# Kernel tuning notes

Hardware: AMD Instinct MI355X
Metric: run time of the kernel (lower is better)

Reference implementation:

```python
import jax, jax.numpy as jnp
import numpy as np

N = 50000
E = 1_600_000


def spmm(edge_index, edge_weight, support, num_nodes):
    # adj[i, j] = w for (i=row, j=col); out[i] = sum_j adj[i,j] * support[j]
    row, col = edge_index[0], edge_index[1]
    msgs = support[col] * edge_weight[:, None]  # [E, d] gather + scale
    return jax.ops.segment_sum(msgs, row, num_segments=num_nodes)


def setup_inputs() -> dict:
    key = jax.random.key(0)
    ks = jax.random.split(key, 7)
    x = jax.random.normal(ks[0], (N, 128), dtype=jnp.float32)
    edge_index = jax.random.randint(ks[1], (2, E), 0, N, dtype=jnp.int64)
    edge_weight = jax.random.uniform(ks[2], (E,), dtype=jnp.float32)
    W1 = jax.random.normal(ks[3], (128, 128), dtype=jnp.float32) * (1.0 / np.sqrt(128))
    b1 = jax.random.normal(ks[4], (128,), dtype=jnp.float32) * (1.0 / np.sqrt(128))
    W2 = jax.random.normal(ks[5], (128, 40), dtype=jnp.float32) * (1.0 / np.sqrt(40))
    b2 = jax.random.normal(ks[6], (40,), dtype=jnp.float32) * (1.0 / np.sqrt(40))
    return {"x": x, "edge_index": edge_index, "edge_weight": edge_weight,
            "W1": W1, "b1": b1, "W2": W2, "b2": b2}


def reference(x, edge_index, edge_weight, W1, b1, W2, b2):
    n = x.shape[0]
    # layer 1: GraphConvolution + ReLU (dropout p=0.0 -> no-op)
    h = spmm(edge_index, edge_weight, x @ W1, n) + b1
    h = jax.nn.relu(h)
    # layer 2: GraphConvolution
    out = spmm(edge_index, edge_weight, h @ W2, n) + b2
    return jax.nn.log_softmax(out, axis=1)
```

## Files before the change

### kernel.cpp

```cpp
#include <hip/hip_runtime.h>
#include <hip/hip_fp16.h>
#include <math.h>

#define N_NODES 50000
#define N_EDGES 1600000
#define D1 128
#define D2 40
#define D2P 48
#define BROWS 128
#define NB 391
#define CHUNK 6250

typedef __attribute__((ext_vector_type(8))) short bf16x8;
typedef __attribute__((ext_vector_type(4))) float f32x4;

__device__ __forceinline__ void bf16_split(float v, unsigned short& h, unsigned short& l) {
    unsigned u = __float_as_uint(v);
    unsigned r = u + 0x7fffu + ((u >> 16) & 1u);
    h = (unsigned short)(r >> 16);
    float hf = __uint_as_float((unsigned)h << 16);
    float lof = v - hf;
    unsigned u2 = __float_as_uint(lof);
    unsigned r2 = u2 + 0x7fffu + ((u2 >> 16) & 1u);
    l = (unsigned short)(r2 >> 16);
}

__device__ __forceinline__ int edge_row(const unsigned int* ei, int e, int is64) {
    return (int)(is64 ? ei[2 * e] : ei[e]);
}
__device__ __forceinline__ int edge_col(const unsigned int* ei, int e, int is64) {
    return (int)(is64 ? ei[2 * (N_EDGES + e)] : ei[N_EDGES + e]);
}

__global__ __launch_bounds__(256) void setup_k(const unsigned int* __restrict__ ei,
                                               int* __restrict__ flag,
                                               unsigned int* __restrict__ gbhp,
                                               const float* __restrict__ W1,
                                               unsigned short* __restrict__ wh1,
                                               unsigned short* __restrict__ wl1,
                                               const float* __restrict__ W2,
                                               unsigned short* __restrict__ wh2,
                                               unsigned short* __restrict__ wl2) {
    int b = blockIdx.x, t = threadIdx.x;
    if (b == 0) {
        __shared__ int any;
        if (t == 0) any = 0;
        __syncthreads();
        for (int i = t; i < 2048; i += 256) {
            if (ei[2 * i + 1] != 0u) any = 1;
        }
        __syncthreads();
        if (t == 0) flag[0] = any ? 0 : 1;
    } else if (b <= 25) {
        int i = (b - 1) * 256 + t;
        if (i < NB * 16) gbhp[i] = 0u;
    } else if (b <= 89) {
        int idx = (b - 26) * 256 + t;
        int k = idx >> 7, n = idx & 127;
        unsigned short h, l;
        bf16_split(W1[k * 128 + n], h, l);
        int nt = n >> 4, ks = k >> 5;
        int lane = (n & 15) | (((k >> 3) & 3) << 4);
        int j = k & 7;
        int dst = ((nt * 4 + ks) * 64 + lane) * 8 + j;
        wh1[dst] = h;
        wl1[dst] = l;
    } else {
        int idx = (b - 90) * 256 + t;
        if (idx < 128 * D2P) {
            int k = idx / D2P, n = idx % D2P;
            float v = (n < D2) ? W2[k * D2 + n] : 0.f;
            unsigned short h, l;
            bf16_split(v, h, l);
            int nt = n >> 4, ks = k >> 5;
            int lane = (n & 15) | (((k >> 3) & 3) << 4);
            int j = k & 7;
            int dst = ((nt * 4 + ks) * 64 + lane) * 8 + j;
            wh2[dst] = h;
            wl2[dst] = l;
        }
    }
}

__global__ __launch_bounds__(256) void bhist_k(const unsigned int* __restrict__ ei,
                                               const int* __restrict__ flag,
                                               unsigned int* __restrict__ gbhp) {
    __shared__ unsigned int bh[NB];
    int is64 = flag[0];
    int t = threadIdx.x;
    for (int i = t; i < NB; i += 256) bh[i] = 0;
    __syncthreads();
    int e0 = blockIdx.x * CHUNK, e1 = e0 + CHUNK;
    for (int e = e0 + t; e < e1; e += 256) {
        atomicAdd(&bh[edge_row(ei, e, is64) >> 7], 1u);
    }
    __syncthreads();
    for (int i = t; i < NB; i += 256) {
        if (bh[i]) atomicAdd(&gbhp[i * 16], bh[i]);
    }
}

__global__ __launch_bounds__(512) void bscan_k(const unsigned int* __restrict__ gbhp,
                                               int* __restrict__ bbase,
                                               unsigned int* __restrict__ bcurp) {
    __shared__ unsigned int s[512];
    int t = threadIdx.x;
    unsigned int v = (t < NB) ? gbhp[t * 16] : 0u;
    s[t] = v;
    __syncthreads();
    for (int off = 1; off < 512; off <<= 1) {
        unsigned int add = (t >= off) ? s[t - off] : 0u;
        __syncthreads();
        s[t] += add;
        __syncthreads();
    }
    if (t < NB) {
        unsigned int excl = s[t] - v;
        bbase[t] = (int)excl;
        bcurp[t * 16] = excl;
    }
    if (t == NB - 1) bbase[NB] = (int)s[t];
}

__global__ __launch_bounds__(256) void bin_k(const unsigned int* __restrict__ ei,
                                             const float* __restrict__ ew,
                                             const int* __restrict__ flag,
                                             unsigned int* __restrict__ bcurp,
                                             uint2* __restrict__ tmp8) {
    __shared__ unsigned int lh[NB];
    __shared__ unsigned int lcur[NB];
    int is64 = flag[0];
    int t = threadIdx.x;
    for (int i = t; i < NB; i += 256) lh[i] = 0;
    __syncthreads();
    int e0 = blockIdx.x * CHUNK, e1 = e0 + CHUNK;
    for (int e = e0 + t; e < e1; e += 256) {
        atomicAdd(&lh[edge_row(ei, e, is64) >> 7], 1u);
    }
    __syncthreads();
    for (int i = t; i < NB; i += 256) {
        if (lh[i]) lcur[i] = atomicAdd(&bcurp[i * 16], lh[i]);
    }
    __syncthreads();
    for (int e = e0 + t; e < e1; e += 256) {
        int r = edge_row(ei, e, is64);
        int c = edge_col(ei, e, is64);
        int b = r >> 7;
        unsigned int p = atomicAdd(&lcur[b], 1u);
        uint2 rec;
        rec.x = ((unsigned int)(r & 127) << 24) | (unsigned int)c;
        rec.y = __float_as_uint(ew[e]);
        tmp8[p] = rec;
    }
}

__global__ __launch_bounds__(256) void csr_k(const uint2* __restrict__ tmp8,
                                             const int* __restrict__ bbase,
                                             int* __restrict__ rowptr,
                                             uint2* __restrict__ colwS) {
    __shared__ unsigned int rcnt[BROWS];
    __shared__ unsigned int loff[BROWS];
    __shared__ unsigned int lcur[BROWS];
    int b = blockIdx.x;
    int t = threadIdx.x;
    int lo = bbase[b], hi = bbase[b + 1];
    int r0 = b * BROWS;
    int nrows = N_NODES - r0;
    if (nrows > BROWS) nrows = BROWS;
    if (t < BROWS) rcnt[t] = 0;
    __syncthreads();
    for (int j = lo + t; j < hi; j += 256) {
        atomicAdd(&rcnt[tmp8[j].x >> 24], 1u);
    }
    __syncthreads();
    if (t < BROWS) loff[t] = rcnt[t];
    __syncthreads();
    for (int off = 1; off < BROWS; off <<= 1) {
        unsigned int add = (t >= off && t < BROWS) ? loff[t - off] : 0u;
        __syncthreads();
        if (t < BROWS) loff[t] += add;
        __syncthreads();
    }
    if (t < BROWS) {
        unsigned int excl = loff[t] - rcnt[t];
        if (t < nrows) rowptr[r0 + t] = lo + (int)excl;
        lcur[t] = (unsigned int)lo + excl;
    }
    if (b == NB - 1 && t == 0) rowptr[N_NODES] = hi;
    __syncthreads();
    for (int j = lo + t; j < hi; j += 256) {
        uint2 rec = tmp8[j];
        unsigned int rl = rec.x >> 24;
        unsigned int p = atomicAdd(&lcur[rl], 1u);
        uint2 cw;
        cw.x = rec.x & 0xFFFFu;
        cw.y = rec.y;
        colwS[p] = cw;
    }
}

__global__ __launch_bounds__(256) void gemm1_k(const float* __restrict__ x,
                                               const unsigned short* __restrict__ wh,
                                               const unsigned short* __restrict__ wl,
                                               __half* __restrict__ Ah) {
    int t = threadIdx.x;
    int w = t >> 6, l = t & 63;
    int row0 = blockIdx.x * 64 + w * 16;
    int arow = row0 + (l & 15);
    if (arow > N_NODES - 1) arow = N_NODES - 1;
    int kbase = (l >> 4) * 8;
    bf16x8 ah[4], al[4];
#pragma unroll
    for (int ks = 0; ks < 4; ++ks) {
        const float* px = &x[arow * D1 + ks * 32 + kbase];
        float4 v0 = *reinterpret_cast<const float4*>(px);
        float4 v1 = *reinterpret_cast<const float4*>(px + 4);
        float vv[8] = {v0.x, v0.y, v0.z, v0.w, v1.x, v1.y, v1.z, v1.w};
#pragma unroll
        for (int j = 0; j < 8; ++j) {
            unsigned short h, lo2;
            bf16_split(vv[j], h, lo2);
            ah[ks][j] = (short)h;
            al[ks][j] = (short)lo2;
        }
    }
    f32x4 acc[8];
#pragma unroll
    for (int nt = 0; nt < 8; ++nt) acc[nt] = (f32x4)(0.f);
#pragma unroll
    for (int nt = 0; nt < 8; ++nt) {
#pragma unroll
        for (int ks = 0; ks < 4; ++ks) {
            int fo = ((nt * 4 + ks) * 64 + l) * 8;
            bf16x8 bh = *reinterpret_cast<const bf16x8*>(&wh[fo]);
            bf16x8 bl = *reinterpret_cast<const bf16x8*>(&wl[fo]);
            acc[nt] = __builtin_amdgcn_mfma_f32_16x16x32_bf16(ah[ks], bh, acc[nt], 0, 0, 0);
            acc[nt] = __builtin_amdgcn_mfma_f32_16x16x32_bf16(ah[ks], bl, acc[nt], 0, 0, 0);
            acc[nt] = __builtin_amdgcn_mfma_f32_16x16x32_bf16(al[ks], bh, acc[nt], 0, 0, 0);
        }
    }
    int crow0 = row0 + (l >> 4) * 4;
    int ccol = l & 15;
#pragma unroll
    for (int nt = 0; nt < 8; ++nt) {
#pragma unroll
        for (int r = 0; r < 4; ++r) {
            int rr = crow0 + r;
            if (rr < N_NODES) Ah[rr * D1 + nt * 16 + ccol] = __float2half_rn(acc[nt][r]);
        }
    }
}

__global__ __launch_bounds__(256) void spmm1_k(const __half* __restrict__ Ah,
                                               const int* __restrict__ rowptr,
                                               const uint2* __restrict__ colwS,
                                               float* __restrict__ B) {
    int t = threadIdx.x;
    int r = blockIdx.x * 4 + (t >> 6);
    int lane = t & 63;
    int half = lane >> 5;
    int cg = lane & 31;
    int s = rowptr[r], e = rowptr[r + 1];
    float4 acc = {0.f, 0.f, 0.f, 0.f};
#pragma unroll 4
    for (int j = s + half; j < e; j += 2) {
        uint2 cw = colwS[j];
        float w = __uint_as_float(cw.y);
        uint2 q = *reinterpret_cast<const uint2*>(&Ah[cw.x * D1 + cg * 4]);
        float2 f0 = __half22float2(*reinterpret_cast<const __half2*>(&q.x));
        float2 f1 = __half22float2(*reinterpret_cast<const __half2*>(&q.y));
        acc.x += w * f0.x;
        acc.y += w * f0.y;
        acc.z += w * f1.x;
        acc.w += w * f1.y;
    }
    acc.x += __shfl_xor(acc.x, 32);
    acc.y += __shfl_xor(acc.y, 32);
    acc.z += __shfl_xor(acc.z, 32);
    acc.w += __shfl_xor(acc.w, 32);
    if (half == 0) *reinterpret_cast<float4*>(&B[r * D1 + cg * 4]) = acc;
}

__global__ __launch_bounds__(256) void gemm2_k(const float* __restrict__ Bm,
                                               const float* __restrict__ b1,
                                               const unsigned short* __restrict__ wh,
                                               const unsigned short* __restrict__ wl,
                                               float* __restrict__ G) {
    int t = threadIdx.x;
    int w = t >> 6, l = t & 63;
    int row0 = blockIdx.x * 64 + w * 16;
    int arow = row0 + (l & 15);
    if (arow > N_NODES - 1) arow = N_NODES - 1;
    int kbase = (l >> 4) * 8;
    bf16x8 ah[4], al[4];
#pragma unroll
    for (int ks = 0; ks < 4; ++ks) {
        const float* pb = &Bm[arow * D1 + ks * 32 + kbase];
        const float* pb1 = &b1[ks * 32 + kbase];
        float4 v0 = *reinterpret_cast<const float4*>(pb);
        float4 v1 = *reinterpret_cast<const float4*>(pb + 4);
        float4 c0 = *reinterpret_cast<const float4*>(pb1);
        float4 c1 = *reinterpret_cast<const float4*>(pb1 + 4);
        float vv[8] = {v0.x + c0.x, v0.y + c0.y, v0.z + c0.z, v0.w + c0.w,
                       v1.x + c1.x, v1.y + c1.y, v1.z + c1.z, v1.w + c1.w};
#pragma unroll
        for (int j = 0; j < 8; ++j) {
            float rv = vv[j] > 0.f ? vv[j] : 0.f;
            unsigned short h, lo2;
            bf16_split(rv, h, lo2);
            ah[ks][j] = (short)h;
            al[ks][j] = (short)lo2;
        }
    }
    f32x4 acc[3];
#pragma unroll
    for (int nt = 0; nt < 3; ++nt) acc[nt] = (f32x4)(0.f);
#pragma unroll
    for (int nt = 0; nt < 3; ++nt) {
#pragma unroll
        for (int ks = 0; ks < 4; ++ks) {
            int fo = ((nt * 4 + ks) * 64 + l) * 8;
            bf16x8 bh = *reinterpret_cast<const bf16x8*>(&wh[fo]);
            bf16x8 bl = *reinterpret_cast<const bf16x8*>(&wl[fo]);
            acc[nt] = __builtin_amdgcn_mfma_f32_16x16x32_bf16(ah[ks], bh, acc[nt], 0, 0, 0);
            acc[nt] = __builtin_amdgcn_mfma_f32_16x16x32_bf16(ah[ks], bl, acc[nt], 0, 0, 0);
            acc[nt] = __builtin_amdgcn_mfma_f32_16x16x32_bf16(al[ks], bh, acc[nt], 0, 0, 0);
        }
    }
    int crow0 = row0 + (l >> 4) * 4;
    int ccol = l & 15;
#pragma unroll
    for (int nt = 0; nt < 3; ++nt) {
        int col = nt * 16 + ccol;
#pragma unroll
        for (int r = 0; r < 4; ++r) {
            int rr = crow0 + r;
            if (rr < N_NODES) G[rr * D2P + col] = acc[nt][r];
        }
    }
}

__global__ __launch_bounds__(256) void spmm2lsm_k(const float* __restrict__ G,
                                                  const int* __restrict__ rowptr,
                                                  const uint2* __restrict__ colwS,
                                                  const float* __restrict__ b2,
                                                  float* __restrict__ out) {
    int t = threadIdx.x;
    int r = blockIdx.x * 4 + (t >> 6);
    int lane = t & 63;
    int slot = lane / 10;
    int comp = lane % 10;
    int s = rowptr[r], e = rowptr[r + 1];
    float4 acc = {0.f, 0.f, 0.f, 0.f};
    bool act = lane < 60;
#pragma unroll 2
    for (int j0 = s; j0 < e; j0 += 6) {
        int j = j0 + slot;
        if (act && j < e) {
            uint2 cw = colwS[j];
            float w = __uint_as_float(cw.y);
            float4 v = *reinterpret_cast<const float4*>(&G[cw.x * D2P + comp * 4]);
            acc.x += w * v.x;
            acc.y += w * v.y;
            acc.z += w * v.z;
            acc.w += w * v.w;
        }
    }
    acc.x += __shfl_down(acc.x, 30);
    acc.y += __shfl_down(acc.y, 30);
    acc.z += __shfl_down(acc.z, 30);
    acc.w += __shfl_down(acc.w, 30);
    {
        float t1 = __shfl_down(acc.x, 10), t2 = __shfl_down(acc.x, 20);
        acc.x += t1 + t2;
        t1 = __shfl_down(acc.y, 10); t2 = __shfl_down(acc.y, 20);
        acc.y += t1 + t2;
        t1 = __shfl_down(acc.z, 10); t2 = __shfl_down(acc.z, 20);
        acc.z += t1 + t2;
        t1 = __shfl_down(acc.w, 10); t2 = __shfl_down(acc.w, 20);
        acc.w += t1 + t2;
    }
    bool valid = lane < 10;
    float4 v4 = {-INFINITY, -INFINITY, -INFINITY, -INFINITY};
    if (valid) {
        float4 bv = *reinterpret_cast<const float4*>(&b2[lane * 4]);
        v4.x = acc.x + bv.x;
        v4.y = acc.y + bv.y;
        v4.z = acc.z + bv.z;
        v4.w = acc.w + bv.w;
    }
    float m = fmaxf(fmaxf(v4.x, v4.y), fmaxf(v4.z, v4.w));
#pragma unroll
    for (int off = 1; off < 16; off <<= 1) m = fmaxf(m, __shfl_xor(m, off));
    float ex = valid ? expf(v4.x - m) + expf(v4.y - m) + expf(v4.z - m) + expf(v4.w - m) : 0.f;
#pragma unroll
    for (int off = 1; off < 16; off <<= 1) ex += __shfl_xor(ex, off);
    float lse = m + logf(ex);
    if (valid) {
        float4 o;
        o.x = v4.x - lse;
        o.y = v4.y - lse;
        o.z = v4.z - lse;
        o.w = v4.w - lse;
        *reinterpret_cast<float4*>(&out[r * D2 + lane * 4]) = o;
    }
}

extern "C" void kernel_launch(void* const* d_in, const int* in_sizes, int n_in,
                              void* d_out, int out_size, void* d_ws, size_t ws_size,
                              hipStream_t stream) {
    const float* x = (const float*)d_in[0];
    const unsigned int* ei = (const unsigned int*)d_in[1];
    const float* ew = (const float*)d_in[2];
    const float* W1 = (const float*)d_in[3];
    const float* b1 = (const float*)d_in[4];
    const float* W2 = (const float*)d_in[5];
    const float* b2 = (const float*)d_in[6];
    float* out = (float*)d_out;

    char* w = (char*)d_ws;
    __half* Ah = (__half*)w;
    float* B = (float*)(w + 12800000);
    uint2* tmp8 = (uint2*)(w + 12800000);
    float* G = (float*)(w + 38400000);
    uint2* colwS = (uint2*)(w + 48000000);
    int* rowptr = (int*)(w + 60800000);
    int* bbase = (int*)(w + 61000832);
    unsigned int* bcurp = (unsigned int*)(w + 61002432);
    unsigned int* gbhp = (unsigned int*)(w + 61027456);
    int* flag = (int*)(w + 61052480);
    unsigned short* wh1 = (unsigned short*)(w + 61052544);
    unsigned short* wl1 = (unsigned short*)(w + 61085312);
    unsigned short* wh2 = (unsigned short*)(w + 61118080);
    unsigned short* wl2 = (unsigned short*)(w + 61130368);

    setup_k<<<114, 256, 0, stream>>>(ei, flag, gbhp, W1, wh1, wl1, W2, wh2, wl2);
    bhist_k<<<256, 256, 0, stream>>>(ei, flag, gbhp);
    bscan_k<<<1, 512, 0, stream>>>(gbhp, bbase, bcurp);
    bin_k<<<256, 256, 0, stream>>>(ei, ew, flag, bcurp, tmp8);
    csr_k<<<NB, 256, 0, stream>>>(tmp8, bbase, rowptr, colwS);

    gemm1_k<<<782, 256, 0, stream>>>(x, wh1, wl1, Ah);
    spmm1_k<<<N_NODES / 4, 256, 0, stream>>>(Ah, rowptr, colwS, B);
    gemm2_k<<<782, 256, 0, stream>>>(B, b1, wh2, wl2, G);
    spmm2lsm_k<<<N_NODES / 4, 256, 0, stream>>>(G, rowptr, colwS, b2, out);
}
```

Baseline: 277.8 us.

## Merge preprocessing kernels, fuse gemm1 with binning, store layer-2 features in fp16

Folds the setup and histogram kernels into one prep kernel. Each block now re-detects the index width itself, and a memset zeroes the histogram. The edge binning and the first dense GEMM share one launch as independent block ranges, which lets them overlap. The second layer's projected features are padded to 64 and stored in fp16, so each gathered row is half the bytes, and the spmm2 lane mapping changes to 4 edges x 16 lanes with shuffled column/weight loads. This cuts launch count and gather traffic, at the cost of fp16 rounding of layer-2 features and redundant detection reads in every block.

```diff
diff --git a/kernel.cpp b/kernel.cpp
--- a/kernel.cpp
+++ b/kernel.cpp
@@ -6,7 +6,7 @@
 #define N_EDGES 1600000
 #define D1 128
 #define D2 40
-#define D2P 48
+#define D2P 64
 #define BROWS 128
 #define NB 391
 #define CHUNK 6250
@@ -25,6 +25,17 @@
     l = (unsigned short)(r2 >> 16);
 }
 
+__device__ __forceinline__ int detect_is64_block(const unsigned int* ei) {
+    __shared__ int any;
+    if (threadIdx.x == 0) any = 0;
+    __syncthreads();
+    int a = 0;
+    for (int i = threadIdx.x; i < 2048; i += 256) a |= (ei[2 * i + 1] != 0u);
+    if (a) any = 1;
+    __syncthreads();
+    return any ? 0 : 1;
+}
+
 __device__ __forceinline__ int edge_row(const unsigned int* ei, int e, int is64) {
     return (int)(is64 ? ei[2 * e] : ei[e]);
 }
@@ -32,30 +43,17 @@
     return (int)(is64 ? ei[2 * (N_EDGES + e)] : ei[N_EDGES + e]);
 }
 
-__global__ __launch_bounds__(256) void setup_k(const unsigned int* __restrict__ ei,
-                                               int* __restrict__ flag,
-                                               unsigned int* __restrict__ gbhp,
-                                               const float* __restrict__ W1,
-                                               unsigned short* __restrict__ wh1,
-                                               unsigned short* __restrict__ wl1,
-                                               const float* __restrict__ W2,
-                                               unsigned short* __restrict__ wh2,
-                                               unsigned short* __restrict__ wl2) {
+__global__ __launch_bounds__(256) void prep_k(const unsigned int* __restrict__ ei,
+                                              unsigned int* __restrict__ gbhp,
+                                              const float* __restrict__ W1,
+                                              unsigned short* __restrict__ wh1,
+                                              unsigned short* __restrict__ wl1,
+                                              const float* __restrict__ W2,
+                                              unsigned short* __restrict__ wh2,
+                                              unsigned short* __restrict__ wl2) {
     int b = blockIdx.x, t = threadIdx.x;
-    if (b == 0) {
-        __shared__ int any;
-        if (t == 0) any = 0;
-        __syncthreads();
-        for (int i = t; i < 2048; i += 256) {
-            if (ei[2 * i + 1] != 0u) any = 1;
-        }
-        __syncthreads();
-        if (t == 0) flag[0] = any ? 0 : 1;
-    } else if (b <= 25) {
-        int i = (b - 1) * 256 + t;
-        if (i < NB * 16) gbhp[i] = 0u;
-    } else if (b <= 89) {
-        int idx = (b - 26) * 256 + t;
+    if (b < 64) {
+        int idx = b * 256 + t;
         int k = idx >> 7, n = idx & 127;
         unsigned short h, l;
         bf16_split(W1[k * 128 + n], h, l);
@@ -65,38 +63,31 @@
         int dst = ((nt * 4 + ks) * 64 + lane) * 8 + j;
         wh1[dst] = h;
         wl1[dst] = l;
+    } else if (b < 96) {
+        int idx = (b - 64) * 256 + t;
+        int k = idx >> 6, n = idx & 63;
+        float v = (n < D2) ? W2[k * D2 + n] : 0.f;
+        unsigned short h, l;
+        bf16_split(v, h, l);
+        int nt = n >> 4, ks = k >> 5;
+        int lane = (n & 15) | (((k >> 3) & 3) << 4);
+        int j = k & 7;
+        int dst = ((nt * 4 + ks) * 64 + lane) * 8 + j;
+        wh2[dst] = h;
+        wl2[dst] = l;
     } else {
-        int idx = (b - 90) * 256 + t;
-        if (idx < 128 * D2P) {
-            int k = idx / D2P, n = idx % D2P;
-            float v = (n < D2) ? W2[k * D2 + n] : 0.f;
-            unsigned short h, l;
-            bf16_split(v, h, l);
-            int nt = n >> 4, ks = k >> 5;
-            int lane = (n & 15) | (((k >> 3) & 3) << 4);
-            int j = k & 7;
-            int dst = ((nt * 4 + ks) * 64 + lane) * 8 + j;
-            wh2[dst] = h;
-            wl2[dst] = l;
-        }
-    }
-}
-
-__global__ __launch_bounds__(256) void bhist_k(const unsigned int* __restrict__ ei,
-                                               const int* __restrict__ flag,
-                                               unsigned int* __restrict__ gbhp) {
-    __shared__ unsigned int bh[NB];
-    int is64 = flag[0];
-    int t = threadIdx.x;
-    for (int i = t; i < NB; i += 256) bh[i] = 0;
-    __syncthreads();
-    int e0 = blockIdx.x * CHUNK, e1 = e0 + CHUNK;
-    for (int e = e0 + t; e < e1; e += 256) {
-        atomicAdd(&bh[edge_row(ei, e, is64) >> 7], 1u);
-    }
-    __syncthreads();
-    for (int i = t; i < NB; i += 256) {
-        if (bh[i]) atomicAdd(&gbhp[i * 16], bh[i]);
+        int is64 = detect_is64_block(ei);
+        __shared__ unsigned int bh[NB];
+        for (int i = t; i < NB; i += 256) bh[i] = 0;
+        __syncthreads();
+        int e0 = (b - 96) * CHUNK, e1 = e0 + CHUNK;
+        for (int e = e0 + t; e < e1; e += 256) {
+            atomicAdd(&bh[edge_row(ei, e, is64) >> 7], 1u);
+        }
+        __syncthreads();
+        for (int i = t; i < NB; i += 256) {
+            if (bh[i]) atomicAdd(&gbhp[i * 16], bh[i]);
+        }
     }
 }
 
@@ -122,35 +113,87 @@
     if (t == NB - 1) bbase[NB] = (int)s[t];
 }
 
-__global__ __launch_bounds__(256) void bin_k(const unsigned int* __restrict__ ei,
-                                             const float* __restrict__ ew,
-                                             const int* __restrict__ flag,
-                                             unsigned int* __restrict__ bcurp,
-                                             uint2* __restrict__ tmp8) {
-    __shared__ unsigned int lh[NB];
-    __shared__ unsigned int lcur[NB];
-    int is64 = flag[0];
-    int t = threadIdx.x;
-    for (int i = t; i < NB; i += 256) lh[i] = 0;
-    __syncthreads();
-    int e0 = blockIdx.x * CHUNK, e1 = e0 + CHUNK;
-    for (int e = e0 + t; e < e1; e += 256) {
-        atomicAdd(&lh[edge_row(ei, e, is64) >> 7], 1u);
-    }
-    __syncthreads();
-    for (int i = t; i < NB; i += 256) {
-        if (lh[i]) lcur[i] = atomicAdd(&bcurp[i * 16], lh[i]);
-    }
-    __syncthreads();
-    for (int e = e0 + t; e < e1; e += 256) {
-        int r = edge_row(ei, e, is64);
-        int c = edge_col(ei, e, is64);
-        int b = r >> 7;
-        unsigned int p = atomicAdd(&lcur[b], 1u);
-        uint2 rec;
-        rec.x = ((unsigned int)(r & 127) << 24) | (unsigned int)c;
-        rec.y = __float_as_uint(ew[e]);
-        tmp8[p] = rec;
+__global__ __launch_bounds__(256) void work1_k(const unsigned int* __restrict__ ei,
+                                               const float* __restrict__ ew,
+                                               unsigned int* __restrict__ bcurp,
+                                               uint2* __restrict__ tmp8,
+                                               const float* __restrict__ x,
+                                               const unsigned short* __restrict__ wh,
+                                               const unsigned short* __restrict__ wl,
+                                               __half* __restrict__ Ah) {
+    int b = blockIdx.x, t = threadIdx.x;
+    if (b < 256) {
+        int is64 = detect_is64_block(ei);
+        __shared__ unsigned int lh[NB];
+        __shared__ unsigned int lcur[NB];
+        for (int i = t; i < NB; i += 256) lh[i] = 0;
+        __syncthreads();
+        int e0 = b * CHUNK, e1 = e0 + CHUNK;
+        for (int e = e0 + t; e < e1; e += 256) {
+            atomicAdd(&lh[edge_row(ei, e, is64) >> 7], 1u);
+        }
+        __syncthreads();
+        for (int i = t; i < NB; i += 256) {
+            if (lh[i]) lcur[i] = atomicAdd(&bcurp[i * 16], lh[i]);
+        }
+        __syncthreads();
+        for (int e = e0 + t; e < e1; e += 256) {
+            int r = edge_row(ei, e, is64);
+            int c = edge_col(ei, e, is64);
+            int bk = r >> 7;
+            unsigned int p = atomicAdd(&lcur[bk], 1u);
+            uint2 rec;
+            rec.x = ((unsigned int)(r & 127) << 24) | (unsigned int)c;
+            rec.y = __float_as_uint(ew[e]);
+            tmp8[p] = rec;
+        }
+    } else {
+        int gb = b - 256;
+        int w = t >> 6, l = t & 63;
+        int row0 = gb * 64 + w * 16;
+        int arow = row0 + (l & 15);
+        if (arow > N_NODES - 1) arow = N_NODES - 1;
+        int kbase = (l >> 4) * 8;
+        bf16x8 ah[4], al[4];
+#pragma unroll
+        for (int ks = 0; ks < 4; ++ks) {
+            const float* px = &x[arow * D1 + ks * 32 + kbase];
+            float4 v0 = *reinterpret_cast<const float4*>(px);
+            float4 v1 = *reinterpret_cast<const float4*>(px + 4);
+            float vv[8] = {v0.x, v0.y, v0.z, v0.w, v1.x, v1.y, v1.z, v1.w};
+#pragma unroll
+            for (int j = 0; j < 8; ++j) {
+                unsigned short h, lo2;
+                bf16_split(vv[j], h, lo2);
+                ah[ks][j] = (short)h;
+                al[ks][j] = (short)lo2;
+            }
+        }
+        f32x4 acc[8];
+#pragma unroll
+        for (int nt = 0; nt < 8; ++nt) acc[nt] = (f32x4)(0.f);
+#pragma unroll
+        for (int nt = 0; nt < 8; ++nt) {
+#pragma unroll
+            for (int ks = 0; ks < 4; ++ks) {
+                int fo = ((nt * 4 + ks) * 64 + l) * 8;
+                bf16x8 bh = *reinterpret_cast<const bf16x8*>(&wh[fo]);
+                bf16x8 bl = *reinterpret_cast<const bf16x8*>(&wl[fo]);
+                acc[nt] = __builtin_amdgcn_mfma_f32_16x16x32_bf16(ah[ks], bh, acc[nt], 0, 0, 0);
+                acc[nt] = __builtin_amdgcn_mfma_f32_16x16x32_bf16(ah[ks], bl, acc[nt], 0, 0, 0);
+                acc[nt] = __builtin_amdgcn_mfma_f32_16x16x32_bf16(al[ks], bh, acc[nt], 0, 0, 0);
+            }
+        }
+        int crow0 = row0 + (l >> 4) * 4;
+        int ccol = l & 15;
+#pragma unroll
+        for (int nt = 0; nt < 8; ++nt) {
+#pragma unroll
+            for (int r = 0; r < 4; ++r) {
+                int rr = crow0 + r;
+                if (rr < N_NODES) Ah[rr * D1 + nt * 16 + ccol] = __float2half_rn(acc[nt][r]);
+            }
+        }
     }
 }
 
@@ -196,58 +239,6 @@
         cw.x = rec.x & 0xFFFFu;
         cw.y = rec.y;
         colwS[p] = cw;
-    }
-}
-
-__global__ __launch_bounds__(256) void gemm1_k(const float* __restrict__ x,
-                                               const unsigned short* __restrict__ wh,
-                                               const unsigned short* __restrict__ wl,
-                                               __half* __restrict__ Ah) {
-    int t = threadIdx.x;
-    int w = t >> 6, l = t & 63;
-    int row0 = blockIdx.x * 64 + w * 16;
-    int arow = row0 + (l & 15);
-    if (arow > N_NODES - 1) arow = N_NODES - 1;
-    int kbase = (l >> 4) * 8;
-    bf16x8 ah[4], al[4];
-#pragma unroll
-    for (int ks = 0; ks < 4; ++ks) {
-        const float* px = &x[arow * D1 + ks * 32 + kbase];
-        float4 v0 = *reinterpret_cast<const float4*>(px);
-        float4 v1 = *reinterpret_cast<const float4*>(px + 4);
-        float vv[8] = {v0.x, v0.y, v0.z, v0.w, v1.x, v1.y, v1.z, v1.w};
-#pragma unroll
-        for (int j = 0; j < 8; ++j) {
-            unsigned short h, lo2;
-            bf16_split(vv[j], h, lo2);
-            ah[ks][j] = (short)h;
-            al[ks][j] = (short)lo2;
-        }
-    }
-    f32x4 acc[8];
-#pragma unroll
-    for (int nt = 0; nt < 8; ++nt) acc[nt] = (f32x4)(0.f);
-#pragma unroll
-    for (int nt = 0; nt < 8; ++nt) {
-#pragma unroll
-        for (int ks = 0; ks < 4; ++ks) {
-            int fo = ((nt * 4 + ks) * 64 + l) * 8;
-            bf16x8 bh = *reinterpret_cast<const bf16x8*>(&wh[fo]);
-            bf16x8 bl = *reinterpret_cast<const bf16x8*>(&wl[fo]);
-            acc[nt] = __builtin_amdgcn_mfma_f32_16x16x32_bf16(ah[ks], bh, acc[nt], 0, 0, 0);
-            acc[nt] = __builtin_amdgcn_mfma_f32_16x16x32_bf16(ah[ks], bl, acc[nt], 0, 0, 0);
-            acc[nt] = __builtin_amdgcn_mfma_f32_16x16x32_bf16(al[ks], bh, acc[nt], 0, 0, 0);
-        }
-    }
-    int crow0 = row0 + (l >> 4) * 4;
-    int ccol = l & 15;
-#pragma unroll
-    for (int nt = 0; nt < 8; ++nt) {
-#pragma unroll
-        for (int r = 0; r < 4; ++r) {
-            int rr = crow0 + r;
-            if (rr < N_NODES) Ah[rr * D1 + nt * 16 + ccol] = __float2half_rn(acc[nt][r]);
-        }
     }
 }
 
@@ -285,7 +276,7 @@
                                                const float* __restrict__ b1,
                                                const unsigned short* __restrict__ wh,
                                                const unsigned short* __restrict__ wl,
-                                               float* __restrict__ G) {
+                                               __half* __restrict__ Gh) {
     int t = threadIdx.x;
     int w = t >> 6, l = t & 63;
     int row0 = blockIdx.x * 64 + w * 16;
@@ -312,11 +303,11 @@
             al[ks][j] = (short)lo2;
         }
     }
-    f32x4 acc[3];
-#pragma unroll
-    for (int nt = 0; nt < 3; ++nt) acc[nt] = (f32x4)(0.f);
-#pragma unroll
-    for (int nt = 0; nt < 3; ++nt) {
+    f32x4 acc[4];
+#pragma unroll
+    for (int nt = 0; nt < 4; ++nt) acc[nt] = (f32x4)(0.f);
+#pragma unroll
+    for (int nt = 0; nt < 4; ++nt) {
 #pragma unroll
         for (int ks = 0; ks < 4; ++ks) {
             int fo = ((nt * 4 + ks) * 64 + l) * 8;
@@ -330,17 +321,17 @@
     int crow0 = row0 + (l >> 4) * 4;
     int ccol = l & 15;
 #pragma unroll
-    for (int nt = 0; nt < 3; ++nt) {
+    for (int nt = 0; nt < 4; ++nt) {
         int col = nt * 16 + ccol;
 #pragma unroll
         for (int r = 0; r < 4; ++r) {
             int rr = crow0 + r;
-            if (rr < N_NODES) G[rr * D2P + col] = acc[nt][r];
-        }
-    }
-}
-
-__global__ __launch_bounds__(256) void spmm2lsm_k(const float* __restrict__ G,
+            if (rr < N_NODES) Gh[rr * D2P + col] = __float2half_rn(acc[nt][r]);
+        }
+    }
+}
+
+__global__ __launch_bounds__(256) void spmm2lsm_k(const __half* __restrict__ Gh,
                                                   const int* __restrict__ rowptr,
                                                   const uint2* __restrict__ colwS,
                                                   const float* __restrict__ b2,
@@ -348,42 +339,38 @@
     int t = threadIdx.x;
     int r = blockIdx.x * 4 + (t >> 6);
     int lane = t & 63;
-    int slot = lane / 10;
-    int comp = lane % 10;
+    int slot = lane >> 4;
+    int li = lane & 15;
     int s = rowptr[r], e = rowptr[r + 1];
     float4 acc = {0.f, 0.f, 0.f, 0.f};
-    bool act = lane < 60;
 #pragma unroll 2
-    for (int j0 = s; j0 < e; j0 += 6) {
+    for (int j0 = s; j0 < e; j0 += 4) {
+        uint2 cwv = colwS[min(j0 + (lane & 3), e - 1)];
         int j = j0 + slot;
-        if (act && j < e) {
-            uint2 cw = colwS[j];
-            float w = __uint_as_float(cw.y);
-            float4 v = *reinterpret_cast<const float4*>(&G[cw.x * D2P + comp * 4]);
-            acc.x += w * v.x;
-            acc.y += w * v.y;
-            acc.z += w * v.z;
-            acc.w += w * v.w;
-        }
-    }
-    acc.x += __shfl_down(acc.x, 30);
-    acc.y += __shfl_down(acc.y, 30);
-    acc.z += __shfl_down(acc.z, 30);
-    acc.w += __shfl_down(acc.w, 30);
-    {
-        float t1 = __shfl_down(acc.x, 10), t2 = __shfl_down(acc.x, 20);
-        acc.x += t1 + t2;
-        t1 = __shfl_down(acc.y, 10); t2 = __shfl_down(acc.y, 20);
-        acc.y += t1 + t2;
-        t1 = __shfl_down(acc.z, 10); t2 = __shfl_down(acc.z, 20);
-        acc.z += t1 + t2;
-        t1 = __shfl_down(acc.w, 10); t2 = __shfl_down(acc.w, 20);
-        acc.w += t1 + t2;
-    }
-    bool valid = lane < 10;
+        if (j < e) {
+            unsigned cx = __shfl(cwv.x, slot);
+            float wv = __uint_as_float(__shfl(cwv.y, slot));
+            uint2 q = reinterpret_cast<const uint2*>(&Gh[cx * D2P])[li];
+            float2 f0 = __half22float2(*reinterpret_cast<const __half2*>(&q.x));
+            float2 f1 = __half22float2(*reinterpret_cast<const __half2*>(&q.y));
+            acc.x += wv * f0.x;
+            acc.y += wv * f0.y;
+            acc.z += wv * f1.x;
+            acc.w += wv * f1.y;
+        }
+    }
+    acc.x += __shfl_down(acc.x, 32);
+    acc.y += __shfl_down(acc.y, 32);
+    acc.z += __shfl_down(acc.z, 32);
+    acc.w += __shfl_down(acc.w, 32);
+    acc.x += __shfl_down(acc.x, 16);
+    acc.y += __shfl_down(acc.y, 16);
+    acc.z += __shfl_down(acc.z, 16);
+    acc.w += __shfl_down(acc.w, 16);
+    bool valid = (lane < 16) && (li < 10);
     float4 v4 = {-INFINITY, -INFINITY, -INFINITY, -INFINITY};
     if (valid) {
-        float4 bv = *reinterpret_cast<const float4*>(&b2[lane * 4]);
+        float4 bv = *reinterpret_cast<const float4*>(&b2[li * 4]);
         v4.x = acc.x + bv.x;
         v4.y = acc.y + bv.y;
         v4.z = acc.z + bv.z;
@@ -402,7 +389,7 @@
         o.y = v4.y - lse;
         o.z = v4.z - lse;
         o.w = v4.w - lse;
-        *reinterpret_cast<float4*>(&out[r * D2 + lane * 4]) = o;
+        *reinterpret_cast<float4*>(&out[r * D2 + li * 4]) = o;
     }
 }
 
@@ -422,26 +409,24 @@
     __half* Ah = (__half*)w;
     float* B = (float*)(w + 12800000);
     uint2* tmp8 = (uint2*)(w + 12800000);
-    float* G = (float*)(w + 38400000);
-    uint2* colwS = (uint2*)(w + 48000000);
-    int* rowptr = (int*)(w + 60800000);
-    int* bbase = (int*)(w + 61000832);
-    unsigned int* bcurp = (unsigned int*)(w + 61002432);
-    unsigned int* gbhp = (unsigned int*)(w + 61027456);
-    int* flag = (int*)(w + 61052480);
-    unsigned short* wh1 = (unsigned short*)(w + 61052544);
-    unsigned short* wl1 = (unsigned short*)(w + 61085312);
-    unsigned short* wh2 = (unsigned short*)(w + 61118080);
-    unsigned short* wl2 = (unsigned short*)(w + 61130368);
-
-    setup_k<<<114, 256, 0, stream>>>(ei, flag, gbhp, W1, wh1, wl1, W2, wh2, wl2);
-    bhist_k<<<256, 256, 0, stream>>>(ei, flag, gbhp);
+    __half* Gh = (__half*)(w + 38400000);
+    uint2* colwS = (uint2*)(w + 44800000);
+    int* rowptr = (int*)(w + 57600000);
+    int* bbase = (int*)(w + 57800064);
+    unsigned int* bcurp = (unsigned int*)(w + 57801664);
+    unsigned int* gbhp = (unsigned int*)(w + 57826688);
+    unsigned short* wh1 = (unsigned short*)(w + 57851712);
+    unsigned short* wl1 = (unsigned short*)(w + 57884480);
+    unsigned short* wh2 = (unsigned short*)(w + 57917248);
+    unsigned short* wl2 = (unsigned short*)(w + 57933632);
+
+    hipMemsetAsync(gbhp, 0, NB * 64, stream);
+    prep_k<<<352, 256, 0, stream>>>(ei, gbhp, W1, wh1, wl1, W2, wh2, wl2);
     bscan_k<<<1, 512, 0, stream>>>(gbhp, bbase, bcurp);
-    bin_k<<<256, 256, 0, stream>>>(ei, ew, flag, bcurp, tmp8);
+    work1_k<<<1038, 256, 0, stream>>>(ei, ew, bcurp, tmp8, x, wh1, wl1, Ah);
     csr_k<<<NB, 256, 0, stream>>>(tmp8, bbase, rowptr, colwS);
 
-    gemm1_k<<<782, 256, 0, stream>>>(x, wh1, wl1, Ah);
     spmm1_k<<<N_NODES / 4, 256, 0, stream>>>(Ah, rowptr, colwS, B);
-    gemm2_k<<<782, 256, 0, stream>>>(B, b1, wh2, wl2, G);
-    spmm2lsm_k<<<N_NODES / 4, 256, 0, stream>>>(G, rowptr, colwS, b2, out);
-}
+    gemm2_k<<<782, 256, 0, stream>>>(B, b1, wh2, wl2, Gh);
+    spmm2lsm_k<<<N_NODES / 4, 256, 0, stream>>>(Gh, rowptr, colwS, b2, out);
+}
```

Measured after the change: 276.4 us. About the same (-0.5%).
